# Kernel optimization log

Hardware: AMD Instinct MI355X
Metric: run time of the kernel (lower is better)

## Reference

```python
import jax, jax.numpy as jnp
import numpy as np

E, B, DS, DA, H = 8, 16384, 32, 8, 128
SLOPE = 0.01  # torch leaky_relu default


def setup_inputs() -> dict:
    key = jax.random.key(0)
    ks = jax.random.split(key, 6)
    din = DS + DA
    return {
        "states": jax.random.normal(ks[0], (E, B, DS), jnp.float32),
        "actions": jax.random.normal(ks[1], (E, B, DA), jnp.float32),
        "W0": jax.random.normal(ks[2], (E, din, H), jnp.float32) / np.sqrt(din),
        "b0": jnp.zeros((E, H), jnp.float32),
        "W1": jax.random.normal(ks[3], (E, H, H), jnp.float32) / np.sqrt(H),
        "b1": jnp.zeros((E, H), jnp.float32),
        "W2": jax.random.normal(ks[4], (E, H, DS), jnp.float32) / np.sqrt(H),
        "b2": jnp.zeros((E, DS), jnp.float32),
    }


def reference(states, actions, W0, b0, W1, b1, W2, b2):
    # inp: (E_in, B, din); each input slice i is evaluated by every member j
    inp = jnp.concatenate([states, actions], axis=2)
    h = jax.nn.leaky_relu(
        jnp.einsum("ibd,jdh->ijbh", inp, W0) + b0[None, :, None, :], SLOPE
    )
    h = jax.nn.leaky_relu(
        jnp.einsum("ijbh,jhk->ijbk", h, W1) + b1[None, :, None, :], SLOPE
    )
    preds = jnp.einsum("ijbh,jhk->ijbk", h, W2) + b2[None, :, None, :]  # (E,E,B,DS)
    delta_mean = preds.mean(axis=0)           # (E, B, DS)
    var = preds.var(axis=0, ddof=1)           # torch.var default is unbiased
    next_state_mean = delta_mean + states
    return next_state_mean, var
```

## Files before the change

### kernel.cpp

```cpp
#include <hip/hip_runtime.h>
#include <hip/hip_fp16.h>


#define NE 8
#define NB 16384
#define DS 32
#define DA 8
#define HH 128
#define DIN 40
#define BT 64
#define NSLOT 96
#define SLOPE 0.01f

using h16x8 = __attribute__((ext_vector_type(8))) _Float16;
using f16x2 = __attribute__((ext_vector_type(2))) _Float16;
using f32x4 = __attribute__((ext_vector_type(4))) float;

__device__ __forceinline__ f16x2 cvtpk(float a, float b) {
    auto r = __builtin_amdgcn_cvt_pkrtz(a, b);
    union { decltype(r) i; f16x2 o; } cv; cv.i = r; return cv.o;
}

__device__ __forceinline__ unsigned int pkh(float a, float b) {
    union { f16x2 h; unsigned int u; } cv;
    cv.h = cvtpk(a, b);
    return cv.u;
}

__device__ __forceinline__ unsigned int pklr(float a, float b) {
    f16x2 z = cvtpk(a, b);
    f16x2 s = z * (_Float16)SLOPE;
    f16x2 r = __builtin_elementwise_max(z, s);
    union { f16x2 h; unsigned int u; } cv; cv.h = r; return cv.u;
}

__device__ __forceinline__ int sin_idx(int row, int kb) {
    return row * 64 + ((kb ^ (row & 7)) << 3);
}
__device__ __forceinline__ int sh_idx(int row, int kb) {
    return row * 128 + ((kb ^ (row & 15)) << 3);
}

__global__ __launch_bounds__(256, 3)
void ens_mlp_kernel(const float* __restrict__ states,
                    const float* __restrict__ actions,
                    const float* __restrict__ W0g,
                    const float* __restrict__ b0g,
                    const float* __restrict__ W1g,
                    const float* __restrict__ b1g,
                    const float* __restrict__ W2g,
                    const float* __restrict__ b2g,
                    float* __restrict__ out)
{
    __shared__ __align__(16) unsigned short sIn[BT * 64];
    __shared__ __align__(16) unsigned short sHa[BT * 128];
    __shared__ __align__(16) unsigned short sHb[BT * 128];

    const int j    = blockIdx.x & 7;
    const int slot = blockIdx.x >> 3;
    const int tid  = threadIdx.x;
    const int wave = tid >> 6;
    const int lane = tid & 63;
    const int q    = lane >> 4;
    const int l16  = lane & 15;
    const int fb   = 32 * wave;
    const int l2m  = 32 * (wave >> 1);
    const int l2n  = 16 * (wave & 1);

    {
        uint4 z; z.x = z.y = z.z = z.w = 0u;
        uint4* p = reinterpret_cast<uint4*>(&sIn[tid * 32]);
        p[0] = z; p[1] = z; p[2] = z; p[3] = z;
    }

    const float* W0j = W0g + j * (DIN * HH);
    const float* W1j = W1g + j * (HH * HH);
    const float* W2j = W2g + j * (HH * DS);

    h16x8 w0f[2][2];
    h16x8 w1f[4][2];
    h16x8 w2f[4];
    f32x4 b0v[2], b1v[2];
    float b2s;

    #pragma unroll
    for (int ks = 0; ks < 2; ++ks)
      #pragma unroll
      for (int mt = 0; mt < 2; ++mt) {
        const int n = fb + mt * 16 + l16;
        #pragma unroll
        for (int t = 0; t < 8; ++t) {
          const int k = ks * 32 + q * 8 + t;
          w0f[ks][mt][t] = (_Float16)((k < DIN) ? W0j[k * HH + n] : 0.f);
        }
      }
    #pragma unroll
    for (int ks = 0; ks < 4; ++ks)
      #pragma unroll
      for (int mt = 0; mt < 2; ++mt) {
        const int n = fb + mt * 16 + l16;
        #pragma unroll
        for (int t = 0; t < 8; ++t) {
          const int k = ks * 32 + q * 8 + t;
          w1f[ks][mt][t] = (_Float16)W1j[k * HH + n];
        }
      }
    #pragma unroll
    for (int ks = 0; ks < 4; ++ks) {
        const int n = l2n + l16;
        #pragma unroll
        for (int t = 0; t < 8; ++t) {
          const int k = ks * 32 + q * 8 + t;
          w2f[ks][t] = (_Float16)W2j[k * DS + n];
        }
    }
    #pragma unroll
    for (int mt = 0; mt < 2; ++mt)
      #pragma unroll
      for (int r = 0; r < 4; ++r) {
        b0v[mt][r] = b0g[j * HH + fb + mt * 16 + q * 4 + r];
        b1v[mt][r] = b1g[j * HH + fb + mt * 16 + q * 4 + r];
      }
    b2s = b2g[j * DS + l2n + l16];

    const f32x4 z4 = {0.f, 0.f, 0.f, 0.f};

    const int srow = tid >> 2;
    const int scb  = tid & 3;
    const int soff = srow * DS + scb * 8;
    unsigned short* const sdst = &sIn[sin_idx(srow, scb)];
    unsigned short* const adst = &sIn[sin_idx(lane, 4)];

    for (int bt = slot; bt < NB / BT; bt += NSLOT) {
        const int b0 = bt * BT;

        {
            const float4* sp = reinterpret_cast<const float4*>(
                states + (size_t)b0 * DS + soff);
            const float4 f0 = sp[0], f1 = sp[1];
            uint4 pk;
            pk.x = pkh(f0.x, f0.y); pk.y = pkh(f0.z, f0.w);
            pk.z = pkh(f1.x, f1.y); pk.w = pkh(f1.z, f1.w);
            *reinterpret_cast<uint4*>(sdst) = pk;
            if (tid < BT) {
                const float4* ap = reinterpret_cast<const float4*>(
                    actions + ((size_t)b0 + lane) * DA);
                const float4 a0 = ap[0], a1 = ap[1];
                uint4 apk;
                apk.x = pkh(a0.x, a0.y); apk.y = pkh(a0.z, a0.w);
                apk.z = pkh(a1.x, a1.y); apk.w = pkh(a1.z, a1.w);
                *reinterpret_cast<uint4*>(adst) = apk;
            }
        }
        __syncthreads();

        float sa[2][4], sq[2][4];
        #pragma unroll
        for (int mt = 0; mt < 2; ++mt)
          #pragma unroll
          for (int r = 0; r < 4; ++r) { sa[mt][r] = 0.f; sq[mt][r] = 0.f; }

        for (int i = 0; i < NE; ++i) {
            #pragma unroll
            for (int nh = 0; nh < 2; ++nh) {
                f32x4 acc[2][2];
                #pragma unroll
                for (int mt = 0; mt < 2; ++mt)
                  #pragma unroll
                  for (int nt = 0; nt < 2; ++nt) acc[mt][nt] = b0v[mt];
                #pragma unroll
                for (int ks = 0; ks < 2; ++ks) {
                    h16x8 bf[2];
                    #pragma unroll
                    for (int nt = 0; nt < 2; ++nt) {
                        const int row = nh * 32 + nt * 16 + l16;
                        bf[nt] = *(const h16x8*)(&sIn[sin_idx(row, ks * 4 + q)]);
                    }
                    #pragma unroll
                    for (int mt = 0; mt < 2; ++mt)
                      #pragma unroll
                      for (int nt = 0; nt < 2; ++nt)
                        acc[mt][nt] = __builtin_amdgcn_mfma_f32_16x16x32_f16(
                            w0f[ks][mt], bf[nt], acc[mt][nt], 0, 0, 0);
                }
                #pragma unroll
                for (int mt = 0; mt < 2; ++mt)
                  #pragma unroll
                  for (int nt = 0; nt < 2; ++nt) {
                    const int row = nh * 32 + nt * 16 + l16;
                    const int blk = (fb >> 3) + mt * 2 + (q >> 1);
                    const int idx = sh_idx(row, blk) + (q & 1) * 4;
                    uint2 pk;
                    pk.x = pklr(acc[mt][nt][0], acc[mt][nt][1]);
                    pk.y = pklr(acc[mt][nt][2], acc[mt][nt][3]);
                    *reinterpret_cast<uint2*>(&sHa[idx]) = pk;
                  }
            }
            __syncthreads();

            if (i < NE - 1) {
                const float4* sp = reinterpret_cast<const float4*>(
                    states + ((size_t)(i + 1) * NB + b0) * DS + soff);
                const float4 f0 = sp[0], f1 = sp[1];
                uint4 pk;
                pk.x = pkh(f0.x, f0.y); pk.y = pkh(f0.z, f0.w);
                pk.z = pkh(f1.x, f1.y); pk.w = pkh(f1.z, f1.w);
                *reinterpret_cast<uint4*>(sdst) = pk;
                if (tid < BT) {
                    const float4* ap = reinterpret_cast<const float4*>(
                        actions + ((size_t)(i + 1) * NB + b0 + lane) * DA);
                    const float4 a0 = ap[0], a1 = ap[1];
                    uint4 apk;
                    apk.x = pkh(a0.x, a0.y); apk.y = pkh(a0.z, a0.w);
                    apk.z = pkh(a1.x, a1.y); apk.w = pkh(a1.z, a1.w);
                    *reinterpret_cast<uint4*>(adst) = apk;
                }
            }

            #pragma unroll
            for (int nh = 0; nh < 2; ++nh) {
                f32x4 acc[2][2];
                #pragma unroll
                for (int mt = 0; mt < 2; ++mt)
                  #pragma unroll
                  for (int nt = 0; nt < 2; ++nt) acc[mt][nt] = b1v[mt];
                #pragma unroll
                for (int ks = 0; ks < 4; ++ks) {
                    h16x8 bf[2];
                    #pragma unroll
                    for (int nt = 0; nt < 2; ++nt) {
                        const int row = nh * 32 + nt * 16 + l16;
                        bf[nt] = *(const h16x8*)(&sHa[sh_idx(row, ks * 4 + q)]);
                    }
                    #pragma unroll
                    for (int mt = 0; mt < 2; ++mt)
                      #pragma unroll
                      for (int nt = 0; nt < 2; ++nt)
                        acc[mt][nt] = __builtin_amdgcn_mfma_f32_16x16x32_f16(
                            w1f[ks][mt], bf[nt], acc[mt][nt], 0, 0, 0);
                }
                #pragma unroll
                for (int mt = 0; mt < 2; ++mt)
                  #pragma unroll
                  for (int nt = 0; nt < 2; ++nt) {
                    const int row = nh * 32 + nt * 16 + l16;
                    const int blk = (fb >> 3) + mt * 2 + (q >> 1);
                    const int idx = sh_idx(row, blk) + (q & 1) * 4;
                    uint2 pk;
                    pk.x = pklr(acc[mt][nt][0], acc[mt][nt][1]);
                    pk.y = pklr(acc[mt][nt][2], acc[mt][nt][3]);
                    *reinterpret_cast<uint2*>(&sHb[idx]) = pk;
                  }
            }
            __syncthreads();

            {
                f32x4 acc2[2];
                acc2[0] = z4; acc2[1] = z4;
                #pragma unroll
                for (int ks = 0; ks < 4; ++ks) {
                    #pragma unroll
                    for (int mt = 0; mt < 2; ++mt) {
                        const int row = l2m + 16 * mt + l16;
                        const h16x8 a2 = *(const h16x8*)(&sHb[sh_idx(row, ks * 4 + q)]);
                        acc2[mt] = __builtin_amdgcn_mfma_f32_16x16x32_f16(
                            a2, w2f[ks], acc2[mt], 0, 0, 0);
                    }
                }
                #pragma unroll
                for (int mt = 0; mt < 2; ++mt)
                  #pragma unroll
                  for (int r = 0; r < 4; ++r) {
                    const float a = acc2[mt][r];
                    sa[mt][r] += a;
                    sq[mt][r] = fmaf(a, a, sq[mt][r]);
                  }
            }
        }

        #pragma unroll
        for (int mt = 0; mt < 2; ++mt)
          #pragma unroll
          for (int r = 0; r < 4; ++r) {
            const int row = l2m + 16 * mt + q * 4 + r;
            const int col = l2n + l16;
            const size_t o = ((size_t)j * NB + b0 + row) * DS + col;
            const float b  = b2s;
            const float s  = sa[mt][r] + 8.f * b;
            const float s2 = sq[mt][r] + 2.f * b * sa[mt][r] + 8.f * b * b;
            out[o] = s * 0.125f + states[o];
            out[(size_t)NE * NB * DS + o] = (s2 - s * s * 0.125f) * (1.0f / 7.0f);
          }
    }
}

extern "C" void kernel_launch(void* const* d_in, const int* in_sizes, int n_in,
                              void* d_out, int out_size, void* d_ws, size_t ws_size,
                              hipStream_t stream) {
    (void)in_sizes; (void)n_in; (void)d_ws; (void)ws_size; (void)out_size;
    const float* states  = (const float*)d_in[0];
    const float* actions = (const float*)d_in[1];
    const float* W0 = (const float*)d_in[2];
    const float* b0 = (const float*)d_in[3];
    const float* W1 = (const float*)d_in[4];
    const float* b1 = (const float*)d_in[5];
    const float* W2 = (const float*)d_in[6];
    const float* b2 = (const float*)d_in[7];
    float* out = (float*)d_out;
    dim3 grid(8 * NSLOT);
    ens_mlp_kernel<<<grid, dim3(256), 0, stream>>>(states, actions, W0, b0, W1, b1, W2, b2, out);
}
```

Measured before the change: 144.8 us.

## Load layer-0 inputs directly into MFMA fragments, drop shared input staging

```diff
diff --git a/kernel.cpp b/kernel.cpp
--- a/kernel.cpp
+++ b/kernel.cpp
@@ -9,7 +9,7 @@
 #define HH 128
 #define DIN 40
 #define BT 64
-#define NSLOT 96
+#define NSLOT 128
 #define SLOPE 0.01f
 
 using h16x8 = __attribute__((ext_vector_type(8))) _Float16;
@@ -21,10 +21,11 @@
     union { decltype(r) i; f16x2 o; } cv; cv.i = r; return cv.o;
 }
 
-__device__ __forceinline__ unsigned int pkh(float a, float b) {
-    union { f16x2 h; unsigned int u; } cv;
-    cv.h = cvtpk(a, b);
-    return cv.u;
+__device__ __forceinline__ h16x8 pack8(float4 a, float4 b) {
+    union { f16x2 h[4]; h16x8 v; } u;
+    u.h[0] = cvtpk(a.x, a.y); u.h[1] = cvtpk(a.z, a.w);
+    u.h[2] = cvtpk(b.x, b.y); u.h[3] = cvtpk(b.z, b.w);
+    return u.v;
 }
 
 __device__ __forceinline__ unsigned int pklr(float a, float b) {
@@ -34,9 +35,6 @@
     union { f16x2 h; unsigned int u; } cv; cv.h = r; return cv.u;
 }
 
-__device__ __forceinline__ int sin_idx(int row, int kb) {
-    return row * 64 + ((kb ^ (row & 7)) << 3);
-}
 __device__ __forceinline__ int sh_idx(int row, int kb) {
     return row * 128 + ((kb ^ (row & 15)) << 3);
 }
@@ -52,7 +50,6 @@
                     const float* __restrict__ b2g,
                     float* __restrict__ out)
 {
-    __shared__ __align__(16) unsigned short sIn[BT * 64];
     __shared__ __align__(16) unsigned short sHa[BT * 128];
     __shared__ __align__(16) unsigned short sHb[BT * 128];
 
@@ -67,12 +64,6 @@
     const int l2m  = 32 * (wave >> 1);
     const int l2n  = 16 * (wave & 1);
 
-    {
-        uint4 z; z.x = z.y = z.z = z.w = 0u;
-        uint4* p = reinterpret_cast<uint4*>(&sIn[tid * 32]);
-        p[0] = z; p[1] = z; p[2] = z; p[3] = z;
-    }
-
     const float* W0j = W0g + j * (DIN * HH);
     const float* W1j = W1g + j * (HH * HH);
     const float* W2j = W2g + j * (HH * DS);
@@ -125,34 +116,8 @@
 
     const f32x4 z4 = {0.f, 0.f, 0.f, 0.f};
 
-    const int srow = tid >> 2;
-    const int scb  = tid & 3;
-    const int soff = srow * DS + scb * 8;
-    unsigned short* const sdst = &sIn[sin_idx(srow, scb)];
-    unsigned short* const adst = &sIn[sin_idx(lane, 4)];
-
     for (int bt = slot; bt < NB / BT; bt += NSLOT) {
         const int b0 = bt * BT;
-
-        {
-            const float4* sp = reinterpret_cast<const float4*>(
-                states + (size_t)b0 * DS + soff);
-            const float4 f0 = sp[0], f1 = sp[1];
-            uint4 pk;
-            pk.x = pkh(f0.x, f0.y); pk.y = pkh(f0.z, f0.w);
-            pk.z = pkh(f1.x, f1.y); pk.w = pkh(f1.z, f1.w);
-            *reinterpret_cast<uint4*>(sdst) = pk;
-            if (tid < BT) {
-                const float4* ap = reinterpret_cast<const float4*>(
-                    actions + ((size_t)b0 + lane) * DA);
-                const float4 a0 = ap[0], a1 = ap[1];
-                uint4 apk;
-                apk.x = pkh(a0.x, a0.y); apk.y = pkh(a0.z, a0.w);
-                apk.z = pkh(a1.x, a1.y); apk.w = pkh(a1.z, a1.w);
-                *reinterpret_cast<uint4*>(adst) = apk;
-            }
-        }
-        __syncthreads();
 
         float sa[2][4], sq[2][4];
         #pragma unroll
@@ -161,28 +126,42 @@
           for (int r = 0; r < 4; ++r) { sa[mt][r] = 0.f; sq[mt][r] = 0.f; }
 
         for (int i = 0; i < NE; ++i) {
+            const float* Si = states  + ((size_t)i * NB + b0) * DS;
+            const float* Ai = actions + ((size_t)i * NB + b0) * DA;
+
             #pragma unroll
             for (int nh = 0; nh < 2; ++nh) {
+                h16x8 bf0[2], bf1[2];
+                #pragma unroll
+                for (int nt = 0; nt < 2; ++nt) {
+                    const int row = nh * 32 + nt * 16 + l16;
+                    const float4* sp = reinterpret_cast<const float4*>(
+                        Si + row * DS + q * 8);
+                    bf0[nt] = pack8(sp[0], sp[1]);
+                    h16x8 za;
+                    #pragma unroll
+                    for (int t = 0; t < 8; ++t) za[t] = (_Float16)0.f;
+                    if (q == 0) {
+                        const float4* ap = reinterpret_cast<const float4*>(
+                            Ai + row * DA);
+                        za = pack8(ap[0], ap[1]);
+                    }
+                    bf1[nt] = za;
+                }
                 f32x4 acc[2][2];
                 #pragma unroll
                 for (int mt = 0; mt < 2; ++mt)
                   #pragma unroll
                   for (int nt = 0; nt < 2; ++nt) acc[mt][nt] = b0v[mt];
                 #pragma unroll
-                for (int ks = 0; ks < 2; ++ks) {
-                    h16x8 bf[2];
-                    #pragma unroll
-                    for (int nt = 0; nt < 2; ++nt) {
-                        const int row = nh * 32 + nt * 16 + l16;
-                        bf[nt] = *(const h16x8*)(&sIn[sin_idx(row, ks * 4 + q)]);
-                    }
-                    #pragma unroll
-                    for (int mt = 0; mt < 2; ++mt)
-                      #pragma unroll
-                      for (int nt = 0; nt < 2; ++nt)
-                        acc[mt][nt] = __builtin_amdgcn_mfma_f32_16x16x32_f16(
-                            w0f[ks][mt], bf[nt], acc[mt][nt], 0, 0, 0);
-                }
+                for (int mt = 0; mt < 2; ++mt)
+                  #pragma unroll
+                  for (int nt = 0; nt < 2; ++nt) {
+                    acc[mt][nt] = __builtin_amdgcn_mfma_f32_16x16x32_f16(
+                        w0f[0][mt], bf0[nt], acc[mt][nt], 0, 0, 0);
+                    acc[mt][nt] = __builtin_amdgcn_mfma_f32_16x16x32_f16(
+                        w0f[1][mt], bf1[nt], acc[mt][nt], 0, 0, 0);
+                  }
                 #pragma unroll
                 for (int mt = 0; mt < 2; ++mt)
                   #pragma unroll
@@ -197,25 +176,6 @@
                   }
             }
             __syncthreads();
-
-            if (i < NE - 1) {
-                const float4* sp = reinterpret_cast<const float4*>(
-                    states + ((size_t)(i + 1) * NB + b0) * DS + soff);
-                const float4 f0 = sp[0], f1 = sp[1];
-                uint4 pk;
-                pk.x = pkh(f0.x, f0.y); pk.y = pkh(f0.z, f0.w);
-                pk.z = pkh(f1.x, f1.y); pk.w = pkh(f1.z, f1.w);
-                *reinterpret_cast<uint4*>(sdst) = pk;
-                if (tid < BT) {
-                    const float4* ap = reinterpret_cast<const float4*>(
-                        actions + ((size_t)(i + 1) * NB + b0 + lane) * DA);
-                    const float4 a0 = ap[0], a1 = ap[1];
-                    uint4 apk;
-                    apk.x = pkh(a0.x, a0.y); apk.y = pkh(a0.z, a0.w);
-                    apk.z = pkh(a1.x, a1.y); apk.w = pkh(a1.z, a1.w);
-                    *reinterpret_cast<uint4*>(adst) = apk;
-                }
-            }
 
             #pragma unroll
             for (int nh = 0; nh < 2; ++nh) {
```

Measured after the change: 205.8 us. 1.42x slower.
